# Optimization experiments

Measured on AMD Instinct MI355X. Metric: run time of the kernel, lower is better.

The kernel has to match this reference:

```python
import jax, jax.numpy as jnp
import numpy as np

SEQ_D = 1024   # sequence_state_dim
PAIR_D = 128   # pairwise_state_dim
H_SEQ = 32     # sequence heads (SEQ_D // 32)
HW = 32        # sequence head width
INNER = PAIR_D // 2  # SequenceToPair inner dim
B, L = 1, 512


def ln(x, g, b):
    m = jnp.mean(x, axis=-1, keepdims=True)
    v = jnp.var(x, axis=-1, keepdims=True)
    return (x - m) * jax.lax.rsqrt(v + 1e-5) * g + b


def setup_inputs() -> dict:
    key = jax.random.key(0)
    ks = jax.random.split(key, 24)
    rn = lambda k, shape, s=0.02: (jax.random.normal(k, shape, jnp.float32) * s)
    inp = {
        "sequence_state": jax.random.normal(ks[0], (B, L, SEQ_D), jnp.float32),
        "pairwise_state": jax.random.normal(ks[1], (B, L, L, PAIR_D), jnp.float32),
        # PairToSequence
        "ln_p2s_g": jnp.ones(PAIR_D), "ln_p2s_b": jnp.zeros(PAIR_D),
        "W_p2s": rn(ks[2], (H_SEQ, PAIR_D)),
        # layernorm_1
        "ln1_g": jnp.ones(SEQ_D), "ln1_b": jnp.zeros(SEQ_D),
        # Attention (gated)
        "Wqkv": rn(ks[3], (3 * SEQ_D, SEQ_D)),
        "Wo": rn(ks[4], (SEQ_D, SEQ_D)), "bo": jnp.zeros(SEQ_D),
        "Wg": rn(ks[5], (SEQ_D, SEQ_D)), "bg": jnp.ones(SEQ_D),
        # mlp_seq
        "ln_s_g": jnp.ones(SEQ_D), "ln_s_b": jnp.zeros(SEQ_D),
        "Wm1": rn(ks[6], (4 * SEQ_D, SEQ_D)), "bm1": jnp.zeros(4 * SEQ_D),
        "Wm2": rn(ks[7], (SEQ_D, 4 * SEQ_D)), "bm2": jnp.zeros(SEQ_D),
        # SequenceToPair
        "ln_sp_g": jnp.ones(SEQ_D), "ln_sp_b": jnp.zeros(SEQ_D),
        "Wsp": rn(ks[8], (2 * INNER, SEQ_D)), "bsp": jnp.zeros(2 * INNER),
        "Wspo": rn(ks[9], (PAIR_D, 2 * INNER)), "bspo": jnp.zeros(PAIR_D),
        # mlp_pair
        "ln_mp_g": jnp.ones(PAIR_D), "ln_mp_b": jnp.zeros(PAIR_D),
        "Wp1": rn(ks[10], (4 * PAIR_D, PAIR_D)), "bp1": jnp.zeros(4 * PAIR_D),
        "Wp2": rn(ks[11], (PAIR_D, 4 * PAIR_D)), "bp2": jnp.zeros(PAIR_D),
        "mask": jnp.ones((B, L), bool),
    }
    return inp


def reference(sequence_state, pairwise_state,
              ln_p2s_g, ln_p2s_b, W_p2s,
              ln1_g, ln1_b, Wqkv, Wo, bo, Wg, bg,
              ln_s_g, ln_s_b, Wm1, bm1, Wm2, bm2,
              ln_sp_g, ln_sp_b, Wsp, bsp, Wspo, bspo,
              ln_mp_g, ln_mp_b, Wp1, bp1, Wp2, bp2,
              mask):
    b, l, _ = sequence_state.shape
    # PairToSequence: pairwise bias  (B, L, L, H)
    bias = ln(pairwise_state, ln_p2s_g, ln_p2s_b) @ W_p2s.T

    # Gated self-attention with pairwise bias
    y = ln(sequence_state, ln1_g, ln1_b)
    t = (y @ Wqkv.T).reshape(b, l, H_SEQ, 3 * HW).transpose(0, 2, 1, 3)  # b h l 3c
    q, k, v = jnp.split(t, 3, axis=-1)
    a = jnp.einsum('bhqc,bhkc->bhqk', q * (HW ** -0.5), k)
    a = a + bias.transpose(0, 3, 1, 2)            # bias: b lq lk h -> b h lq lk
    a = jnp.where(mask[:, None, None, :], a, -jnp.inf)
    a = jax.nn.softmax(a, axis=-1)
    o = jnp.einsum('bhqk,bhkc->bqhc', a, v).reshape(b, l, SEQ_D)
    o = jax.nn.sigmoid(y @ Wg.T + bg) * o         # gate computed from layernormed input
    o = o @ Wo.T + bo
    s = sequence_state + o

    # mlp_seq residual
    s = s + (jax.nn.relu(ln(s, ln_s_g, ln_s_b) @ Wm1.T + bm1) @ Wm2.T + bm2)

    # SequenceToPair: outer-product-style pair update
    sp = ln(s, ln_sp_g, ln_sp_b) @ Wsp.T + bsp    # b l 2*inner
    qh, kh = jnp.split(sp, 2, axis=-1)
    prod = qh[:, None, :, :] * kh[:, :, None, :]  # b l l inner
    diff = qh[:, None, :, :] - kh[:, :, None, :]
    pz = jnp.concatenate([prod, diff], axis=-1) @ Wspo.T + bspo
    p = pairwise_state + pz

    # mlp_pair residual
    p = p + (jax.nn.relu(ln(p, ln_mp_g, ln_mp_b) @ Wp1.T + bp1) @ Wp2.T + bp2)
    return (s, p)
```

## Files before the change

### kernel.cpp

```cpp
#include <hip/hip_runtime.h>
#include <hip/hip_bf16.h>
#include <cstddef>


#define L 512
#define SEQ_D 1024
#define PAIR_D 128
#define NH 32
#define HW 32

typedef short bf16x8 __attribute__((ext_vector_type(8)));
typedef float f32x4 __attribute__((ext_vector_type(4)));
typedef unsigned short ushort_t;

__device__ inline float wred_sum(float v) {
#pragma unroll
  for (int off = 32; off; off >>= 1) v += __shfl_xor(v, off, 64);
  return v;
}
__device__ inline unsigned pk2(float a, float b) {
  unsigned ua = __float_as_uint(a), ub = __float_as_uint(b);
  ua = (ua + 0x7fffu + ((ua >> 16) & 1u)) >> 16;
  ub = (ub + 0x7fffu + ((ub >> 16) & 1u)) >> 16;
  return ua | (ub << 16);
}
__device__ inline ushort_t bf1(float a) {
  unsigned ua = __float_as_uint(a);
  return (ushort_t)((ua + 0x7fffu + ((ua >> 16) & 1u)) >> 16);
}
__device__ inline float bfl(unsigned u) { return __uint_as_float(u << 16); }
__device__ inline float bfh(unsigned u) { return __uint_as_float(u & 0xffff0000u); }
__device__ inline float bfu(ushort_t u) { return __uint_as_float((unsigned)u << 16); }

#define SWZ(row, kb) ((((row)) << 8) + ((kb) ^ (((row)&7) << 4)))
#define SWZ64(row, kb) ((((row)) << 7) + ((kb) ^ (((row)&7) << 4)))

__device__ __forceinline__ void stage_w32k(const ushort_t* __restrict__ src,
                                           int row_stride, int col_off,
                                           char* lds, int w, int l) {
#pragma unroll
  for (int i = 0; i < 8; ++i) {
    const int o = w * 8192 + i * 1024 + l * 16;
    const int row = o >> 8;
    const int kb = (o & 255) ^ (((row) & 7) << 4);
    const ushort_t* g = src + (size_t)row * row_stride + col_off + (kb >> 1);
    __builtin_amdgcn_global_load_lds(
        (const __attribute__((address_space(1))) unsigned int*)g,
        (__attribute__((address_space(3))) unsigned int*)(lds + w * 8192 + i * 1024),
        16, 0, 0);
  }
}

__global__ __launch_bounds__(256) void cvt9_kernel(
    const float* __restrict__ s0, ushort_t* __restrict__ d0,
    const float* __restrict__ s1, ushort_t* __restrict__ d1,
    const float* __restrict__ s2, ushort_t* __restrict__ d2,
    const float* __restrict__ s3, ushort_t* __restrict__ d3,
    const float* __restrict__ s4, ushort_t* __restrict__ d4,
    const float* __restrict__ s5, ushort_t* __restrict__ d5,
    const float* __restrict__ s6, ushort_t* __restrict__ d6,
    const float* __restrict__ s7, ushort_t* __restrict__ d7,
    const float* __restrict__ s8, ushort_t* __restrict__ d8) {
  const int b = blockIdx.x;
  if (b >= 6728) {
    const float* s; ushort_t* d; int base, rowlen;
    if (b < 6760) { s = s7; d = d7; base = b - 6728; rowlen = 128; }
    else          { s = s8; d = d8; base = b - 6760; rowlen = 512; }
    const int i = base * 256 + threadIdx.x;
    float4 a = ((const float4*)s)[2 * i], c = ((const float4*)s)[2 * i + 1];
    const int fe = i * 8;
    const int row = fe / rowlen;
    const int fk = fe % rowlen;
    const int ch = fk >> 7, k0 = fk & 127;
    const int kk = k0 >> 5, r0 = k0 & 31;
    const int hi = (r0 >> 4) & 1, g16a = (r0 >> 2) & 3;
    const int p1 = kk * 32 + g16a * 8 + hi * 4;
    ushort_t* dst = d + (size_t)row * rowlen + ch * 128;
    uint2 w1; w1.x = pk2(a.x, a.y); w1.y = pk2(a.z, a.w);
    uint2 w2; w2.x = pk2(c.x, c.y); w2.y = pk2(c.z, c.w);
    *(uint2*)(dst + p1) = w1;
    *(uint2*)(dst + p1 + 8) = w2;
    return;
  }
  const float* s; ushort_t* d; int base;
  if (b < 1536)      { s = s0; d = d0; base = b; }
  else if (b < 2048) { s = s1; d = d1; base = b - 1536; }
  else if (b < 2560) { s = s2; d = d2; base = b - 2048; }
  else if (b < 4608) { s = s3; d = d3; base = b - 2560; }
  else if (b < 6656) { s = s4; d = d4; base = b - 4608; }
  else if (b < 6720) { s = s5; d = d5; base = b - 6656; }
  else               { s = s6; d = d6; base = b - 6720; }
  const int i = base * 256 + threadIdx.x;
  float4 a = ((const float4*)s)[2 * i], c = ((const float4*)s)[2 * i + 1];
  uint4 w;
  w.x = pk2(a.x, a.y); w.y = pk2(a.z, a.w);
  w.z = pk2(c.x, c.y); w.w = pk2(c.z, c.w);
  ((uint4*)d)[i] = w;
}

__global__ __launch_bounds__(256) void ln1024b_kernel(
    const float* __restrict__ in, const float* __restrict__ g,
    const float* __restrict__ b, ushort_t* __restrict__ out) {
  const int row = blockIdx.x;
  const int tid = threadIdx.x;
  float4 v = ((const float4*)(in + (size_t)row * SEQ_D))[tid];
  float s = v.x + v.y + v.z + v.w;
  float s2 = v.x * v.x + v.y * v.y + v.z * v.z + v.w * v.w;
  __shared__ float red[8];
  const int lane = tid & 63, wid = tid >> 6;
  s = wred_sum(s);
  s2 = wred_sum(s2);
  if (lane == 0) { red[wid] = s; red[4 + wid] = s2; }
  __syncthreads();
  s = red[0] + red[1] + red[2] + red[3];
  s2 = red[4] + red[5] + red[6] + red[7];
  const float mean = s * (1.0f / SEQ_D);
  const float var = s2 * (1.0f / SEQ_D) - mean * mean;
  const float rstd = rsqrtf(var + 1e-5f);
  float4 gv = ((const float4*)g)[tid];
  float4 bv = ((const float4*)b)[tid];
  const float o0 = (v.x - mean) * rstd * gv.x + bv.x;
  const float o1 = (v.y - mean) * rstd * gv.y + bv.y;
  const float o2 = (v.z - mean) * rstd * gv.z + bv.z;
  const float o3 = (v.w - mean) * rstd * gv.w + bv.w;
  uint2 pkd; pkd.x = pk2(o0, o1); pkd.y = pk2(o2, o3);
  ((uint2*)(out + (size_t)row * SEQ_D))[tid] = pkd;
}

template <int BIAS, int RELU, int RES, int OBF16>
__global__ __launch_bounds__(256, 2) void gemm_mfma_kernel(
    const ushort_t* __restrict__ A, const ushort_t* __restrict__ B,
    const float* __restrict__ bias, const float* __restrict__ res,
    float* __restrict__ C, ushort_t* __restrict__ Cb, int M, int N, int K) {
  __shared__ __align__(16) char smem[24576];
  char* Ab = smem;
  char* Bb = smem + 8192;
  const int tid = threadIdx.x;
  const int l = tid & 63, w = tid >> 6;
  const int wr = w >> 1, wc = w & 1;
  const int lane16 = l & 15, g16 = l >> 4;
  const int bm = blockIdx.y * 64, bn = blockIdx.x * 128;
  const f32x4 fz = {0.f, 0.f, 0.f, 0.f};
  f32x4 acc[4][2];
#pragma unroll
  for (int i = 0; i < 4; ++i)
#pragma unroll
    for (int j = 0; j < 2; ++j) acc[i][j] = fz;

  for (int k0 = 0; k0 < K; k0 += 64) {
    __syncthreads();
#pragma unroll
    for (int u = 0; u < 2; ++u) {
      const int slot = u * 256 + tid;
      const int row = slot >> 3, sl = slot & 7;
      bf16x8 v = *(const bf16x8*)(A + (size_t)(bm + row) * K + k0 + sl * 8);
      *(bf16x8*)(Ab + SWZ64(row, sl * 16)) = v;
    }
#pragma unroll
    for (int u = 0; u < 4; ++u) {
      const int slot = u * 256 + tid;
      const int row = slot >> 3, sl = slot & 7;
      bf16x8 v = *(const bf16x8*)(B + (size_t)(bn + row) * K + k0 + sl * 8);
      *(bf16x8*)(Bb + SWZ64(row, sl * 16)) = v;
    }
    __syncthreads();
#pragma unroll
    for (int kk = 0; kk < 2; ++kk) {
      const int kb = kk * 64 + g16 * 16;
      bf16x8 af[2], bf[4];
#pragma unroll
      for (int rb = 0; rb < 2; ++rb) {
        const int row = wr * 32 + rb * 16 + lane16;
        af[rb] = *(const bf16x8*)(Ab + SWZ64(row, kb));
      }
#pragma unroll
      for (int cb = 0; cb < 4; ++cb) {
        const int row = wc * 64 + cb * 16 + lane16;
        bf[cb] = *(const bf16x8*)(Bb + SWZ64(row, kb));
      }
#pragma unroll
      for (int cb = 0; cb < 4; ++cb)
#pragma unroll
        for (int rb = 0; rb < 2; ++rb)
          acc[cb][rb] = __builtin_amdgcn_mfma_f32_16x16x32_bf16(
              bf[cb], af[rb], acc[cb][rb], 0, 0, 0);
    }
  }
#pragma unroll
  for (int cb = 0; cb < 4; ++cb) {
    const int col0 = bn + wc * 64 + cb * 16 + g16 * 4;
    float4 bi = make_float4(0.f, 0.f, 0.f, 0.f);
    if (BIAS) bi = *(const float4*)(bias + col0);
#pragma unroll
    for (int rb = 0; rb < 2; ++rb) {
      const int row = bm + wr * 32 + rb * 16 + lane16;
      f32x4 v = acc[cb][rb];
      v[0] += bi.x; v[1] += bi.y; v[2] += bi.z; v[3] += bi.w;
      if (RELU) {
        v[0] = fmaxf(v[0], 0.f); v[1] = fmaxf(v[1], 0.f);
        v[2] = fmaxf(v[2], 0.f); v[3] = fmaxf(v[3], 0.f);
      }
      if (RES) {
        const float4 r4 = *(const float4*)(res + (size_t)row * N + col0);
        v[0] += r4.x; v[1] += r4.y; v[2] += r4.z; v[3] += r4.w;
      }
      if (OBF16) {
        uint2 pkd; pkd.x = pk2(v[0], v[1]); pkd.y = pk2(v[2], v[3]);
        *(uint2*)(Cb + (size_t)row * N + col0) = pkd;
      } else {
        float4 o4; o4.x = v[0]; o4.y = v[1]; o4.z = v[2]; o4.w = v[3];
        *(float4*)(C + (size_t)row * N + col0) = o4;
      }
    }
  }
}

__global__ __launch_bounds__(256) void p2s_mfma_kernel(
    const float* __restrict__ pair, const float* __restrict__ g,
    const float* __restrict__ b, const float* __restrict__ W,
    ushort_t* __restrict__ biasTb) {
  __shared__ __align__(16) char pnb[32768];
  __shared__ __align__(16) char wls[8192];
  const int tid = threadIdx.x;
  const int l = tid & 63, w = tid >> 6;
  const int lane16 = l & 15, g16 = l >> 4;
  const size_t r0 = (size_t)blockIdx.x * 128;
  const int i_idx = (int)(r0 >> 9), j0 = (int)(r0 & 511);
#pragma unroll
  for (int u = 0; u < 2; ++u) {
    const int slot = u * 256 + tid;
    const int row = slot >> 4, sl = slot & 15;
    const float4 v0 = *(const float4*)(W + (size_t)row * 128 + sl * 8);
    const float4 v1 = *(const float4*)(W + (size_t)row * 128 + sl * 8 + 4);
    uint4 wv; wv.x = pk2(v0.x, v0.y); wv.y = pk2(v0.z, v0.w);
    wv.z = pk2(v1.x, v1.y); wv.w = pk2(v1.z, v1.w);
    *(uint4*)(wls + SWZ(row, sl * 16)) = wv;
  }
  {
    const int l32 = tid & 31, rg = tid >> 5;
    const float4 gv = *(const float4*)(g + l32 * 4);
    const float4 bv = *(const float4*)(b + l32 * 4);
#pragma unroll
    for (int it = 0; it < 16; ++it) {
      const int r = it * 8 + rg;
      const float4 v = *(const float4*)(pair + (r0 + r) * 128 + l32 * 4);
      float s = v.x + v.y + v.z + v.w;
      float s2 = v.x * v.x + v.y * v.y + v.z * v.z + v.w * v.w;
#pragma unroll
      for (int off = 1; off < 32; off <<= 1) {
        s += __shfl_xor(s, off, 64);
        s2 += __shfl_xor(s2, off, 64);
      }
      const float mean = s * (1.0f / 128.0f);
      const float rstd = rsqrtf(s2 * (1.0f / 128.0f) - mean * mean + 1e-5f);
      const float n0 = (v.x - mean) * rstd * gv.x + bv.x;
      const float n1 = (v.y - mean) * rstd * gv.y + bv.y;
      const float n2 = (v.z - mean) * rstd * gv.z + bv.z;
      const float n3 = (v.w - mean) * rstd * gv.w + bv.w;
      uint2 pkd; pkd.x = pk2(n0, n1); pkd.y = pk2(n2, n3);
      *(uint2*)(pnb + SWZ(r, l32 * 8)) = pkd;
    }
  }
  __syncthreads();
  const f32x4 fz = {0.f, 0.f, 0.f, 0.f};
  f32x4 a2[2][2];
#pragma unroll
  for (int i = 0; i < 2; ++i)
#pragma unroll
    for (int j = 0; j < 2; ++j) a2[i][j] = fz;
#pragma unroll
  for (int kk = 0; kk < 4; ++kk) {
    bf16x8 wf[2], pf[2];
#pragma unroll
    for (int hb = 0; hb < 2; ++hb)
      wf[hb] = *(const bf16x8*)(wls + SWZ(hb * 16 + lane16, kk * 64 + g16 * 16));
#pragma unroll
    for (int rb = 0; rb < 2; ++rb)
      pf[rb] = *(const bf16x8*)(pnb + SWZ(w * 32 + rb * 16 + lane16, kk * 64 + g16 * 16));
#pragma unroll
    for (int hb = 0; hb < 2; ++hb)
#pragma unroll
      for (int rb = 0; rb < 2; ++rb)
        a2[hb][rb] = __builtin_amdgcn_mfma_f32_16x16x32_bf16(
            wf[hb], pf[rb], a2[hb][rb], 0, 0, 0);
  }
#pragma unroll
  for (int hb = 0; hb < 2; ++hb)
#pragma unroll
    for (int rb = 0; rb < 2; ++rb) {
      const int j = j0 + w * 32 + rb * 16 + lane16;
#pragma unroll
      for (int qq = 0; qq < 4; ++qq) {
        const int hh = hb * 16 + g16 * 4 + qq;
        biasTb[((size_t)hh * 512 + i_idx) * 512 + j] = bf1(a2[hb][rb][qq]);
      }
    }
}

__global__ __launch_bounds__(256) void attn_kernel(
    const ushort_t* __restrict__ tb, const ushort_t* __restrict__ biasTb,
    const float* __restrict__ gbuf, ushort_t* __restrict__ ob) {
  __shared__ __align__(16) ushort_t Vt[32][80];
  const int tid = threadIdx.x;
  const int l = tid & 63, wq = tid >> 6;
  const int lane16 = l & 15, g16 = l >> 4;
  const int h = blockIdx.y;
  const int q = blockIdx.x * 64 + wq * 16 + lane16;
  const float scale = 0.17677669529663689f;
  const bf16x8 qf = *(const bf16x8*)(tb + (size_t)q * 3072 + h * 96 + g16 * 8);
  const ushort_t* brow = biasTb + ((size_t)h * 512 + q) * 512;
  float m = -3e38f, lsum = 0.f;
  const f32x4 fz = {0.f, 0.f, 0.f, 0.f};
  f32x4 accp[2] = {fz, fz};
  for (int kt = 0; kt < 512; kt += 64) {
    {
      const int kr = tid >> 2, cc = tid & 3;
      bf16x8 vv = *(const bf16x8*)(tb + (size_t)(kt + kr) * 3072 + h * 96 + 64 + cc * 8);
#pragma unroll
      for (int u = 0; u < 8; ++u) Vt[cc * 8 + u][kr] = (ushort_t)vv[u];
    }
    __syncthreads();
    f32x4 st[4];
#pragma unroll
    for (int kb = 0; kb < 4; ++kb) {
      const bf16x8 kf = *(const bf16x8*)(
          tb + (size_t)(kt + kb * 16 + lane16) * 3072 + h * 96 + 32 + g16 * 8);
      st[kb] = __builtin_amdgcn_mfma_f32_16x16x32_bf16(kf, qf, fz, 0, 0, 0);
      const ushort4 bv = *(const ushort4*)(brow + kt + kb * 16 + g16 * 4);
      st[kb][0] = st[kb][0] * scale + bfu(bv.x);
      st[kb][1] = st[kb][1] * scale + bfu(bv.y);
      st[kb][2] = st[kb][2] * scale + bfu(bv.z);
      st[kb][3] = st[kb][3] * scale + bfu(bv.w);
    }
    float tm = st[0][0];
#pragma unroll
    for (int kb = 0; kb < 4; ++kb)
#pragma unroll
      for (int qq = 0; qq < 4; ++qq) tm = fmaxf(tm, st[kb][qq]);
    tm = fmaxf(tm, __shfl_xor(tm, 16, 64));
    tm = fmaxf(tm, __shfl_xor(tm, 32, 64));
    const float mn = fmaxf(m, tm);
    const float corr = __expf(m - mn);
    m = mn;
    lsum *= corr;
#pragma unroll
    for (int ct = 0; ct < 2; ++ct) {
      accp[ct][0] *= corr; accp[ct][1] *= corr;
      accp[ct][2] *= corr; accp[ct][3] *= corr;
    }
#pragma unroll
    for (int kb = 0; kb < 4; ++kb)
#pragma unroll
      for (int qq = 0; qq < 4; ++qq) {
        const float e = __expf(st[kb][qq] - mn);
        st[kb][qq] = e;
        lsum += e;
      }
    const int src0 = lane16 + ((l & 16) << 1);
    const int src1 = src0 + 16;
    const bool hi = (l & 32) != 0;
#pragma unroll
    for (int kk = 0; kk < 2; ++kk) {
      float lo4[4], hi4[4];
#pragma unroll
      for (int qq = 0; qq < 4; ++qq) {
        const float a0 = __shfl(st[kk * 2][qq], src0, 64);
        const float a1 = __shfl(st[kk * 2][qq], src1, 64);
        const float b0 = __shfl(st[kk * 2 + 1][qq], src0, 64);
        const float b1 = __shfl(st[kk * 2 + 1][qq], src1, 64);
        lo4[qq] = hi ? b0 : a0;
        hi4[qq] = hi ? b1 : a1;
      }
      uint4 pu;
      pu.x = pk2(lo4[0], lo4[1]); pu.y = pk2(lo4[2], lo4[3]);
      pu.z = pk2(hi4[0], hi4[1]); pu.w = pk2(hi4[2], hi4[3]);
      bf16x8 pf;
      __builtin_memcpy(&pf, &pu, 16);
#pragma unroll
      for (int ct = 0; ct < 2; ++ct) {
        const bf16x8 vf = *(const bf16x8*)&Vt[ct * 16 + lane16][kk * 32 + g16 * 8];
        accp[ct] = __builtin_amdgcn_mfma_f32_16x16x32_bf16(vf, pf, accp[ct], 0, 0, 0);
      }
    }
    __syncthreads();
  }
  lsum += __shfl_xor(lsum, 16, 64);
  lsum += __shfl_xor(lsum, 32, 64);
  const float inv = 1.0f / lsum;
#pragma unroll
  for (int ct = 0; ct < 2; ++ct) {
    const int col = h * 32 + ct * 16 + g16 * 4;
    const float4 gv = *(const float4*)(gbuf + (size_t)q * SEQ_D + col);
    float4 o4;
    o4.x = accp[ct][0] * inv * (1.0f / (1.0f + __expf(-gv.x)));
    o4.y = accp[ct][1] * inv * (1.0f / (1.0f + __expf(-gv.y)));
    o4.z = accp[ct][2] * inv * (1.0f / (1.0f + __expf(-gv.z)));
    o4.w = accp[ct][3] * inv * (1.0f / (1.0f + __expf(-gv.w)));
    uint2 pkd; pkd.x = pk2(o4.x, o4.y); pkd.y = pk2(o4.z, o4.w);
    *(uint2*)(ob + (size_t)q * SEQ_D + col) = pkd;
  }
}

__global__ __launch_bounds__(256, 2) void pairfuse64_kernel(
    const float* __restrict__ spb, const ushort_t* __restrict__ Wspob,
    const float* __restrict__ bspo, const float* __restrict__ pairw,
    const float* __restrict__ lng, const float* __restrict__ lnb,
    const ushort_t* __restrict__ Wp1b, const float* __restrict__ bp1,
    const ushort_t* __restrict__ Wp2b, const float* __restrict__ bp2,
    float* __restrict__ pout) {
  __shared__ __align__(16) char Wbuf[65536];
  char* buf0 = Wbuf;
  char* buf1 = Wbuf + 32768;
  const int tid = threadIdx.x;
  const int l = tid & 63, w = tid >> 6;
  const int lane16 = l & 15, g16 = l >> 4;
  const size_t r0 = (size_t)blockIdx.x * 128;
  const int i_idx = (int)(r0 >> 9), j0 = (int)(r0 & 511);
  size_t grow[2];
  grow[0] = r0 + w * 32 + lane16;
  grow[1] = grow[0] + 16;

  stage_w32k(Wspob, 128, 0, buf0, w, l);
  stage_w32k(Wp1b, 128, 0, buf1, w, l);

  bf16x8 xf[2][4];
  {
    const float* krow = spb + (size_t)i_idx * 128 + 64;
#pragma unroll
    for (int rb = 0; rb < 2; ++rb) {
      const float* qrow = spb + (size_t)(j0 + w * 32 + rb * 16 + lane16) * 128;
#pragma unroll
      for (int kk = 0; kk < 4; ++kk) {
        const int c = ((kk & 1) << 5) + g16 * 8;
        const float4 q0 = *(const float4*)(qrow + c);
        const float4 q1 = *(const float4*)(qrow + c + 4);
        const float4 k0 = *(const float4*)(krow + c);
        const float4 k1 = *(const float4*)(krow + c + 4);
        uint4 u;
        if (kk < 2) {
          u.x = pk2(q0.x * k0.x, q0.y * k0.y);
          u.y = pk2(q0.z * k0.z, q0.w * k0.w);
          u.z = pk2(q1.x * k1.x, q1.y * k1.y);
          u.w = pk2(q1.z * k1.z, q1.w * k1.w);
        } else {
          u.x = pk2(q0.x - k0.x, q0.y - k0.y);
          u.y = pk2(q0.z - k0.z, q0.w - k0.w);
          u.z = pk2(q1.x - k1.x, q1.y - k1.y);
          u.w = pk2(q1.z - k1.z, q1.w - k1.w);
        }
        __builtin_memcpy(&xf[rb][kk], &u, 16);
      }
    }
  }
  __syncthreads();

  const f32x4 fz = {0.f, 0.f, 0.f, 0.f};
  f32x4 acc[2][8];
#pragma unroll
  for (int rb = 0; rb < 2; ++rb)
#pragma unroll
    for (int cb = 0; cb < 8; ++cb) acc[rb][cb] = fz;
#pragma unroll
  for (int cb = 0; cb < 8; ++cb) {
#pragma unroll
    for (int kk = 0; kk < 4; ++kk) {
      const bf16x8 wf = *(const bf16x8*)(
          buf0 + SWZ(cb * 16 + lane16, kk * 64 + g16 * 16));
      acc[0][cb] = __builtin_amdgcn_mfma_f32_16x16x32_bf16(wf, xf[0][kk], acc[0][cb], 0, 0, 0);
      acc[1][cb] = __builtin_amdgcn_mfma_f32_16x16x32_bf16(wf, xf[1][kk], acc[1][cb], 0, 0, 0);
    }
  }

  uint2 Ppk[2][8];
  bf16x8 pnf[2][4];
#pragma unroll
  for (int rb = 0; rb < 2; ++rb) {
    float s = 0.f, s2 = 0.f;
#pragma unroll
    for (int cb = 0; cb < 8; ++cb) {
      const int col0 = cb * 16 + g16 * 4;
      const float4 bs = *(const float4*)(bspo + col0);
      const float4 pw = *(const float4*)(pairw + grow[rb] * 128 + col0);
      acc[rb][cb][0] += bs.x + pw.x; acc[rb][cb][1] += bs.y + pw.y;
      acc[rb][cb][2] += bs.z + pw.z; acc[rb][cb][3] += bs.w + pw.w;
      s += acc[rb][cb][0] + acc[rb][cb][1] + acc[rb][cb][2] + acc[rb][cb][3];
      s2 += acc[rb][cb][0] * acc[rb][cb][0] + acc[rb][cb][1] * acc[rb][cb][1] +
            acc[rb][cb][2] * acc[rb][cb][2] + acc[rb][cb][3] * acc[rb][cb][3];
      Ppk[rb][cb].x = pk2(acc[rb][cb][0], acc[rb][cb][1]);
      Ppk[rb][cb].y = pk2(acc[rb][cb][2], acc[rb][cb][3]);
    }
    s += __shfl_xor(s, 16, 64);  s += __shfl_xor(s, 32, 64);
    s2 += __shfl_xor(s2, 16, 64); s2 += __shfl_xor(s2, 32, 64);
    const float mean = s * (1.0f / 128.0f);
    const float rstd = rsqrtf(s2 * (1.0f / 128.0f) - mean * mean + 1e-5f);
    uint2 pnpk[8];
#pragma unroll
    for (int cb = 0; cb < 8; ++cb) {
      const int col0 = cb * 16 + g16 * 4;
      const float4 gv = *(const float4*)(lng + col0);
      const float4 bv = *(const float4*)(lnb + col0);
      const float n0 = (acc[rb][cb][0] - mean) * rstd * gv.x + bv.x;
      const float n1 = (acc[rb][cb][1] - mean) * rstd * gv.y + bv.y;
      const float n2 = (acc[rb][cb][2] - mean) * rstd * gv.z + bv.z;
      const float n3 = (acc[rb][cb][3] - mean) * rstd * gv.w + bv.w;
      pnpk[cb].x = pk2(n0, n1); pnpk[cb].y = pk2(n2, n3);
    }
#pragma unroll
    for (int fk = 0; fk < 4; ++fk) {
      uint4 u;
      u.x = pnpk[2 * fk].x;     u.y = pnpk[2 * fk].y;
      u.z = pnpk[2 * fk + 1].x; u.w = pnpk[2 * fk + 1].y;
      __builtin_memcpy(&pnf[rb][fk], &u, 16);
    }
  }

  f32x4 acc2[2][8];
#pragma unroll
  for (int rb = 0; rb < 2; ++rb)
#pragma unroll
    for (int cb = 0; cb < 8; ++cb) acc2[rb][cb] = fz;

  for (int ch = 0; ch < 4; ++ch) {
    __syncthreads();
    stage_w32k(Wp2b, 512, ch * 128, buf0, w, l);
    bf16x8 hf[2][4];
#pragma unroll
    for (int fk = 0; fk < 4; ++fk) {
      uint2 hpk[2][2];
#pragma unroll
      for (int cbl = 0; cbl < 2; ++cbl) {
        const int cb = fk * 2 + cbl;
        f32x4 hacc[2] = {fz, fz};
#pragma unroll
        for (int kk = 0; kk < 4; ++kk) {
          const bf16x8 w1f = *(const bf16x8*)(
              buf1 + SWZ(cb * 16 + lane16, kk * 64 + g16 * 16));
          hacc[0] = __builtin_amdgcn_mfma_f32_16x16x32_bf16(w1f, pnf[0][kk], hacc[0], 0, 0, 0);
          hacc[1] = __builtin_amdgcn_mfma_f32_16x16x32_bf16(w1f, pnf[1][kk], hacc[1], 0, 0, 0);
        }
        const int hcol = ch * 128 + cb * 16 + g16 * 4;
        const float4 bi = *(const float4*)(bp1 + hcol);
#pragma unroll
        for (int rb = 0; rb < 2; ++rb) {
          const float h0 = fmaxf(hacc[rb][0] + bi.x, 0.f);
          const float h1 = fmaxf(hacc[rb][1] + bi.y, 0.f);
          const float h2 = fmaxf(hacc[rb][2] + bi.z, 0.f);
          const float h3 = fmaxf(hacc[rb][3] + bi.w, 0.f);
          hpk[rb][cbl].x = pk2(h0, h1); hpk[rb][cbl].y = pk2(h2, h3);
        }
      }
#pragma unroll
      for (int rb = 0; rb < 2; ++rb) {
        uint4 u;
        u.x = hpk[rb][0].x; u.y = hpk[rb][0].y;
        u.z = hpk[rb][1].x; u.w = hpk[rb][1].y;
        __builtin_memcpy(&hf[rb][fk], &u, 16);
      }
    }
    __syncthreads();
    if (ch < 3) stage_w32k(Wp1b + (size_t)(ch + 1) * 128 * 128, 128, 0, buf1, w, l);
#pragma unroll
    for (int cb = 0; cb < 8; ++cb) {
#pragma unroll
      for (int kk = 0; kk < 4; ++kk) {
        const bf16x8 w2f = *(const bf16x8*)(
            buf0 + SWZ(cb * 16 + lane16, kk * 64 + g16 * 16));
        acc2[0][cb] = __builtin_amdgcn_mfma_f32_16x16x32_bf16(w2f, hf[0][kk], acc2[0][cb], 0, 0, 0);
        acc2[1][cb] = __builtin_amdgcn_mfma_f32_16x16x32_bf16(w2f, hf[1][kk], acc2[1][cb], 0, 0, 0);
      }
    }
  }

#pragma unroll
  for (int rb = 0; rb < 2; ++rb) {
#pragma unroll
    for (int cb = 0; cb < 8; ++cb) {
      const int col0 = cb * 16 + g16 * 4;
      const float4 b2 = *(const float4*)(bp2 + col0);
      float4 o4;
      o4.x = acc2[rb][cb][0] + b2.x + bfl(Ppk[rb][cb].x);
      o4.y = acc2[rb][cb][1] + b2.y + bfh(Ppk[rb][cb].x);
      o4.z = acc2[rb][cb][2] + b2.z + bfl(Ppk[rb][cb].y);
      o4.w = acc2[rb][cb][3] + b2.w + bfh(Ppk[rb][cb].y);
      *(float4*)(pout + grow[rb] * 128 + col0) = o4;
    }
  }
}

extern "C" void kernel_launch(void* const* d_in, const int* in_sizes, int n_in,
                              void* d_out, int out_size, void* d_ws,
                              size_t ws_size, hipStream_t stream) {
  (void)in_sizes; (void)n_in; (void)out_size; (void)ws_size;
  const float* seq      = (const float*)d_in[0];
  const float* pair     = (const float*)d_in[1];
  const float* ln_p2s_g = (const float*)d_in[2];
  const float* ln_p2s_b = (const float*)d_in[3];
  const float* W_p2s    = (const float*)d_in[4];
  const float* ln1_g    = (const float*)d_in[5];
  const float* ln1_b    = (const float*)d_in[6];
  const float* Wqkv     = (const float*)d_in[7];
  const float* Wo       = (const float*)d_in[8];
  const float* bo       = (const float*)d_in[9];
  const float* Wg       = (const float*)d_in[10];
  const float* bg       = (const float*)d_in[11];
  const float* ln_s_g   = (const float*)d_in[12];
  const float* ln_s_b   = (const float*)d_in[13];
  const float* Wm1      = (const float*)d_in[14];
  const float* bm1      = (const float*)d_in[15];
  const float* Wm2      = (const float*)d_in[16];
  const float* bm2      = (const float*)d_in[17];
  const float* ln_sp_g  = (const float*)d_in[18];
  const float* ln_sp_b  = (const float*)d_in[19];
  const float* Wsp      = (const float*)d_in[20];
  const float* bsp      = (const float*)d_in[21];
  const float* Wspo     = (const float*)d_in[22];
  const float* bspo     = (const float*)d_in[23];
  const float* ln_mp_g  = (const float*)d_in[24];
  const float* ln_mp_b  = (const float*)d_in[25];
  const float* Wp1      = (const float*)d_in[26];
  const float* bp1      = (const float*)d_in[27];
  const float* Wp2      = (const float*)d_in[28];
  const float* bp2      = (const float*)d_in[29];

  float* out_s = (float*)d_out;
  float* out_p = out_s + 512 * 1024;

  float* ws = (float*)d_ws;
  ushort_t* y_b = (ushort_t*)ws;
  ushort_t* t_b = (ushort_t*)(ws + 262144);
  float* g   = ws + 1048576;
  float* s1  = g + 524288;
  ushort_t* ob  = (ushort_t*)(s1 + 524288);
  ushort_t* h1b = (ushort_t*)(s1 + 524288 + 262144);
  float* spb = s1 + 524288 + 262144 + 1048576;
  ushort_t* wspo_b = (ushort_t*)(spb + 65536);
  ushort_t* wp1_b  = (ushort_t*)(spb + 65536 + 8192);
  ushort_t* wp2_b  = (ushort_t*)(spb + 65536 + 40960);

  ushort_t* biasTb = (ushort_t*)out_p;
  ushort_t* wq_b  = (ushort_t*)(out_p + 8388608);
  ushort_t* wg_b  = wq_b + 3145728;
  ushort_t* wo_b  = wg_b + 1048576;
  ushort_t* wm1_b = wo_b + 1048576;
  ushort_t* wm2_b = wm1_b + 4194304;
  ushort_t* wsp_b = wm2_b + 4194304;

  cvt9_kernel<<<6792, 256, 0, stream>>>(Wqkv, wq_b, Wg, wg_b, Wo, wo_b,
                                        Wm1, wm1_b, Wm2, wm2_b, Wsp, wsp_b,
                                        Wspo, wspo_b, Wp1, wp1_b, Wp2, wp2_b);
  ln1024b_kernel<<<512, 256, 0, stream>>>(seq, ln1_g, ln1_b, y_b);
  gemm_mfma_kernel<0, 0, 0, 1><<<dim3(24, 8), 256, 0, stream>>>(
      y_b, wq_b, nullptr, nullptr, nullptr, t_b, 512, 3072, 1024);
  gemm_mfma_kernel<1, 0, 0, 0><<<dim3(8, 8), 256, 0, stream>>>(
      y_b, wg_b, bg, nullptr, g, nullptr, 512, 1024, 1024);
  p2s_mfma_kernel<<<2048, 256, 0, stream>>>(pair, ln_p2s_g, ln_p2s_b, W_p2s,
                                            biasTb);
  attn_kernel<<<dim3(8, 32), 256, 0, stream>>>(t_b, biasTb, g, ob);
  gemm_mfma_kernel<1, 0, 1, 0><<<dim3(8, 8), 256, 0, stream>>>(
      ob, wo_b, bo, seq, s1, nullptr, 512, 1024, 1024);
  ln1024b_kernel<<<512, 256, 0, stream>>>(s1, ln_s_g, ln_s_b, y_b);
  gemm_mfma_kernel<1, 1, 0, 1><<<dim3(32, 8), 256, 0, stream>>>(
      y_b, wm1_b, bm1, nullptr, nullptr, h1b, 512, 4096, 1024);
  gemm_mfma_kernel<1, 0, 1, 0><<<dim3(8, 8), 256, 0, stream>>>(
      h1b, wm2_b, bm2, s1, out_s, nullptr, 512, 1024, 4096);
  ln1024b_kernel<<<512, 256, 0, stream>>>(out_s, ln_sp_g, ln_sp_b, y_b);
  gemm_mfma_kernel<1, 0, 0, 0><<<dim3(1, 8), 256, 0, stream>>>(
      y_b, wsp_b, bsp, nullptr, spb, nullptr, 512, 128, 1024);
  pairfuse64_kernel<<<2048, 256, 0, stream>>>(spb, wspo_b, bspo, pair,
                                              ln_mp_g, ln_mp_b, wp1_b, bp1,
                                              wp2_b, bp2, out_p);
}
```

Measured before the change: 412.9 us.

## Fuse QKV and gate projections into one GEMM and use hardware bf16 convert

New measurement: 376.4 us (median of 2 runs). 1.1x faster.

```diff
diff --git a/kernel.cpp b/kernel.cpp
--- a/kernel.cpp
+++ b/kernel.cpp
@@ -19,14 +19,14 @@
   return v;
 }
 __device__ inline unsigned pk2(float a, float b) {
-  unsigned ua = __float_as_uint(a), ub = __float_as_uint(b);
-  ua = (ua + 0x7fffu + ((ua >> 16) & 1u)) >> 16;
-  ub = (ub + 0x7fffu + ((ub >> 16) & 1u)) >> 16;
-  return ua | (ub << 16);
+  unsigned r;
+  asm("v_cvt_pk_bf16_f32 %0, %1, %2" : "=v"(r) : "v"(a), "v"(b));
+  return r;
 }
 __device__ inline ushort_t bf1(float a) {
-  unsigned ua = __float_as_uint(a);
-  return (ushort_t)((ua + 0x7fffu + ((ua >> 16) & 1u)) >> 16);
+  unsigned r;
+  asm("v_cvt_pk_bf16_f32 %0, %1, %2" : "=v"(r) : "v"(a), "v"(0.f));
+  return (ushort_t)r;
 }
 __device__ inline float bfl(unsigned u) { return __uint_as_float(u << 16); }
 __device__ inline float bfh(unsigned u) { return __uint_as_float(u & 0xffff0000u); }
@@ -60,8 +60,14 @@
     const float* __restrict__ s5, ushort_t* __restrict__ d5,
     const float* __restrict__ s6, ushort_t* __restrict__ d6,
     const float* __restrict__ s7, ushort_t* __restrict__ d7,
-    const float* __restrict__ s8, ushort_t* __restrict__ d8) {
+    const float* __restrict__ s8, ushort_t* __restrict__ d8,
+    const float* __restrict__ bgate, float* __restrict__ bias_cat) {
   const int b = blockIdx.x;
+  if (b >= 6792) {
+    const int i = (b - 6792) * 256 + threadIdx.x;
+    bias_cat[i] = (i < 3072) ? 0.f : bgate[i - 3072];
+    return;
+  }
   if (b >= 6728) {
     const float* s; ushort_t* d; int base, rowlen;
     if (b < 6760) { s = s7; d = d7; base = b - 6728; rowlen = 128; }
@@ -299,7 +305,7 @@
 
 __global__ __launch_bounds__(256) void attn_kernel(
     const ushort_t* __restrict__ tb, const ushort_t* __restrict__ biasTb,
-    const float* __restrict__ gbuf, ushort_t* __restrict__ ob) {
+    ushort_t* __restrict__ ob) {
   __shared__ __align__(16) ushort_t Vt[32][80];
   const int tid = threadIdx.x;
   const int l = tid & 63, wq = tid >> 6;
@@ -307,7 +313,7 @@
   const int h = blockIdx.y;
   const int q = blockIdx.x * 64 + wq * 16 + lane16;
   const float scale = 0.17677669529663689f;
-  const bf16x8 qf = *(const bf16x8*)(tb + (size_t)q * 3072 + h * 96 + g16 * 8);
+  const bf16x8 qf = *(const bf16x8*)(tb + (size_t)q * 4096 + h * 96 + g16 * 8);
   const ushort_t* brow = biasTb + ((size_t)h * 512 + q) * 512;
   float m = -3e38f, lsum = 0.f;
   const f32x4 fz = {0.f, 0.f, 0.f, 0.f};
@@ -315,7 +321,7 @@
   for (int kt = 0; kt < 512; kt += 64) {
     {
       const int kr = tid >> 2, cc = tid & 3;
-      bf16x8 vv = *(const bf16x8*)(tb + (size_t)(kt + kr) * 3072 + h * 96 + 64 + cc * 8);
+      bf16x8 vv = *(const bf16x8*)(tb + (size_t)(kt + kr) * 4096 + h * 96 + 64 + cc * 8);
 #pragma unroll
       for (int u = 0; u < 8; ++u) Vt[cc * 8 + u][kr] = (ushort_t)vv[u];
     }
@@ -324,7 +330,7 @@
 #pragma unroll
     for (int kb = 0; kb < 4; ++kb) {
       const bf16x8 kf = *(const bf16x8*)(
-          tb + (size_t)(kt + kb * 16 + lane16) * 3072 + h * 96 + 32 + g16 * 8);
+          tb + (size_t)(kt + kb * 16 + lane16) * 4096 + h * 96 + 32 + g16 * 8);
       st[kb] = __builtin_amdgcn_mfma_f32_16x16x32_bf16(kf, qf, fz, 0, 0, 0);
       const ushort4 bv = *(const ushort4*)(brow + kt + kb * 16 + g16 * 4);
       st[kb][0] = st[kb][0] * scale + bfu(bv.x);
@@ -390,12 +396,12 @@
 #pragma unroll
   for (int ct = 0; ct < 2; ++ct) {
     const int col = h * 32 + ct * 16 + g16 * 4;
-    const float4 gv = *(const float4*)(gbuf + (size_t)q * SEQ_D + col);
+    const ushort4 gv = *(const ushort4*)(tb + (size_t)q * 4096 + 3072 + col);
     float4 o4;
-    o4.x = accp[ct][0] * inv * (1.0f / (1.0f + __expf(-gv.x)));
-    o4.y = accp[ct][1] * inv * (1.0f / (1.0f + __expf(-gv.y)));
-    o4.z = accp[ct][2] * inv * (1.0f / (1.0f + __expf(-gv.z)));
-    o4.w = accp[ct][3] * inv * (1.0f / (1.0f + __expf(-gv.w)));
+    o4.x = accp[ct][0] * inv * (1.0f / (1.0f + __expf(-bfu(gv.x))));
+    o4.y = accp[ct][1] * inv * (1.0f / (1.0f + __expf(-bfu(gv.y))));
+    o4.z = accp[ct][2] * inv * (1.0f / (1.0f + __expf(-bfu(gv.z))));
+    o4.w = accp[ct][3] * inv * (1.0f / (1.0f + __expf(-bfu(gv.w))));
     uint2 pkd; pkd.x = pk2(o4.x, o4.y); pkd.y = pk2(o4.z, o4.w);
     *(uint2*)(ob + (size_t)q * SEQ_D + col) = pkd;
   }
@@ -628,14 +634,14 @@
   float* ws = (float*)d_ws;
   ushort_t* y_b = (ushort_t*)ws;
   ushort_t* t_b = (ushort_t*)(ws + 262144);
-  float* g   = ws + 1048576;
-  float* s1  = g + 524288;
+  float* s1  = ws + 262144 + 1048576;
   ushort_t* ob  = (ushort_t*)(s1 + 524288);
   ushort_t* h1b = (ushort_t*)(s1 + 524288 + 262144);
   float* spb = s1 + 524288 + 262144 + 1048576;
   ushort_t* wspo_b = (ushort_t*)(spb + 65536);
   ushort_t* wp1_b  = (ushort_t*)(spb + 65536 + 8192);
   ushort_t* wp2_b  = (ushort_t*)(spb + 65536 + 40960);
+  float* bias_cat  = spb + 65536 + 73728;
 
   ushort_t* biasTb = (ushort_t*)out_p;
   ushort_t* wq_b  = (ushort_t*)(out_p + 8388608);
@@ -645,17 +651,16 @@
   ushort_t* wm2_b = wm1_b + 4194304;
   ushort_t* wsp_b = wm2_b + 4194304;
 
-  cvt9_kernel<<<6792, 256, 0, stream>>>(Wqkv, wq_b, Wg, wg_b, Wo, wo_b,
+  cvt9_kernel<<<6808, 256, 0, stream>>>(Wqkv, wq_b, Wg, wg_b, Wo, wo_b,
                                         Wm1, wm1_b, Wm2, wm2_b, Wsp, wsp_b,
-                                        Wspo, wspo_b, Wp1, wp1_b, Wp2, wp2_b);
+                                        Wspo, wspo_b, Wp1, wp1_b, Wp2, wp2_b,
+                                        bg, bias_cat);
   ln1024b_kernel<<<512, 256, 0, stream>>>(seq, ln1_g, ln1_b, y_b);
-  gemm_mfma_kernel<0, 0, 0, 1><<<dim3(24, 8), 256, 0, stream>>>(
-      y_b, wq_b, nullptr, nullptr, nullptr, t_b, 512, 3072, 1024);
-  gemm_mfma_kernel<1, 0, 0, 0><<<dim3(8, 8), 256, 0, stream>>>(
-      y_b, wg_b, bg, nullptr, g, nullptr, 512, 1024, 1024);
+  gemm_mfma_kernel<1, 0, 0, 1><<<dim3(32, 8), 256, 0, stream>>>(
+      y_b, wq_b, bias_cat, nullptr, nullptr, t_b, 512, 4096, 1024);
   p2s_mfma_kernel<<<2048, 256, 0, stream>>>(pair, ln_p2s_g, ln_p2s_b, W_p2s,
                                             biasTb);
-  attn_kernel<<<dim3(8, 32), 256, 0, stream>>>(t_b, biasTb, g, ob);
+  attn_kernel<<<dim3(8, 32), 256, 0, stream>>>(t_b, biasTb, ob);
   gemm_mfma_kernel<1, 0, 1, 0><<<dim3(8, 8), 256, 0, stream>>>(
       ob, wo_b, bo, seq, s1, nullptr, 512, 1024, 1024);
   ln1024b_kernel<<<512, 256, 0, stream>>>(s1, ln_s_g, ln_s_b, y_b);
```
